# Kernel optimization log

Measured on AMD Instinct MI355X. Metric: run time of the kernel, lower is better.

## Reference

```python
import jax, jax.numpy as jnp
import numpy as np
import math

B, N, D = 1, 50000, 512  # batch (forced to 1 by the module's matmul shapes), nodes, embed_dim


def _uniform(key, shape, stdv):
    return jax.random.uniform(key, shape, minval=-stdv, maxval=stdv, dtype=jnp.float32)


def setup_inputs() -> dict:
    key = jax.random.key(0)
    ks = jax.random.split(key, 11)
    q = jax.random.normal(ks[0], (B, N, D), dtype=jnp.float32)
    l = jax.random.normal(ks[1], (B, 1, D), dtype=jnp.float32)
    context = jax.random.normal(ks[2], (B, 1, D), dtype=jnp.float32)
    g = jax.random.normal(ks[3], (B, 1, D), dtype=jnp.float32)
    mask = jax.random.randint(ks[4], (B, N), 0, 2, dtype=jnp.int32)
    mask = mask.at[:, 0].set(1)  # guarantee at least one feasible node
    random_net = jax.random.randint(ks[5], (B, 1), 0, N, dtype=jnp.int64)
    # learned parameters, uniform(-1/sqrt(fan), 1/sqrt(fan)) per init_parameters
    W_context = _uniform(ks[6], (1, 1, 2), 1.0 / math.sqrt(2))
    W_graph = _uniform(ks[7], (1, 1, 2), 1.0 / math.sqrt(2))
    W_query = _uniform(ks[8], (D, D), 1.0 / math.sqrt(D))
    W_key = _uniform(ks[9], (D, D), 1.0 / math.sqrt(D))
    return {
        "q": q, "l": l, "context": context, "g": g, "mask": mask,
        "is_random": 0, "random_net": random_net,
        "W_context": W_context, "W_graph": W_graph,
        "W_query": W_query, "W_key": W_key,
    }


def reference(q, l, context, g, mask, is_random, random_net,
              W_context, W_graph, W_query, W_key):
    batch_size, graph_size, input_dim = q.shape
    mask_copy = mask
    norm_factor = 1.0 / math.sqrt(input_dim)  # key_dim == embed_dim (n_heads=1)

    # context mixing: concat = W_context[0] @ [l; context]  -> (B,1,D)
    lc = jnp.concatenate([l, context], axis=1).reshape(-1, input_dim)      # (2B, D)
    concat = jnp.matmul(W_context[0], lc).reshape(batch_size, 1, input_dim)
    # graph mixing: g_context = W_graph[0] @ [g; concat]    -> (B,1,D)
    gc = jnp.concatenate([g, concat], axis=1).reshape(-1, input_dim)
    g_context = jnp.matmul(W_graph[0], gc).reshape(batch_size, 1, input_dim)

    Q = jnp.matmul(g_context.reshape(-1, input_dim), W_query).reshape(batch_size, 1, -1)
    K = jnp.matmul(q.reshape(-1, input_dim), W_key).reshape(batch_size, graph_size, -1)

    compat = jnp.tanh(norm_factor * jnp.einsum('bqk,bnk->bqn', Q, K)) * 10.0  # (B,1,N)
    maskf = mask.astype(jnp.float32)[:, None, :]
    compat = jnp.where(maskf <= 0.1, -jnp.inf, compat)

    softmax = jax.nn.softmax(compat, axis=2)
    log_softmax = jax.nn.log_softmax(compat, axis=2)

    if not is_random:  # static Python branch (is_random is a plain int)
        max_indx = jnp.argmax(softmax, axis=2)          # (B,1)
    else:
        max_indx = random_net

    rows = jnp.arange(batch_size)
    idx = max_indx[:, 0]
    q_max = q[rows, idx][:, None, :]                    # (B,1,D)
    attn_max = softmax[rows, 0, idx].reshape(batch_size, 1)
    log_attn_max = log_softmax[rows, 0, idx].reshape(batch_size, 1)
    return (q_max, attn_max, log_attn_max, concat, mask_copy, max_indx)
```

## Files before the change

kernel.cpp:

```cpp
#include <hip/hip_runtime.h>
#include <math.h>

#define DIM 512
#define NROWS 50000
#define NORM 0.04419417382415922f

#define QP_BLOCKS 64
#define QPART_BLOCKS 32
#define VK_BLOCKS 128
#define CP_BLOCKS 2048
#define CP_THREADS 256

#define OUT_ATTN 512
#define OUT_LOG  513
#define OUT_IDX  51026


__device__ inline float dot4(float4 a, float4 b, float acc) {
    acc = fmaf(a.x, b.x, acc);
    acc = fmaf(a.y, b.y, acc);
    acc = fmaf(a.z, b.z, acc);
    acc = fmaf(a.w, b.w, acc);
    return acc;
}

__device__ inline void sm_combine(float& m, float& s, int& idx,
                                  float m2, float s2, int idx2) {
    bool take2 = (m2 > m) || (m2 == m && idx2 < idx);
    float hm = take2 ? m2 : m;
    float hs = take2 ? s2 : s;
    int   hi = take2 ? idx2 : idx;
    float lm = take2 ? m : m2;
    float ls = take2 ? s : s2;
    if (lm > -INFINITY) hs = fmaf(ls, expf(lm - hm), hs);
    m = hm; s = hs; idx = hi;
}

__global__ __launch_bounds__(256) void qpart_kernel(
    const float* __restrict__ l, const float* __restrict__ ctx,
    const float* __restrict__ g, const float* __restrict__ Wc,
    const float* __restrict__ Wg, const float* __restrict__ Wq,
    const int* __restrict__ mask,
    float* __restrict__ qpart, float* __restrict__ out_concat,
    float* __restrict__ out_maskf) {
    int t = threadIdx.x;
    int b = blockIdx.x;
    for (int i = b * 256 + t; i < NROWS; i += QP_BLOCKS * 256)
        out_maskf[i] = (float)mask[i];
    if (b >= QPART_BLOCKS) return;

    __shared__ float gctx[DIM];
    float wc0 = Wc[0], wc1 = Wc[1], wg0 = Wg[0], wg1 = Wg[1];
    for (int j = t; j < DIM; j += 256) {
        float cc = wc0 * l[j] + wc1 * ctx[j];
        if (b == 0) out_concat[j] = cc;
        gctx[j] = wg0 * g[j] + wg1 * cc;
    }
    __syncthreads();
    int d0 = b * 16;
    float acc0 = 0.f, acc1 = 0.f;
    for (int d = d0; d < d0 + 16; ++d) {
        float gd = gctx[d];
        acc0 = fmaf(gd, Wq[d * DIM + t], acc0);
        acc1 = fmaf(gd, Wq[d * DIM + t + 256], acc1);
    }
    qpart[b * DIM + t] = acc0;
    qpart[b * DIM + t + 256] = acc1;
}

__global__ __launch_bounds__(256) void v_kernel(
    const float* __restrict__ Wk, const float* __restrict__ qpart,
    float* __restrict__ v) {
    __shared__ __align__(16) float Q[DIM];
    int t = threadIdx.x;
    for (int j = t; j < DIM; j += 256) {
        float a = 0.f;
        for (int p = 0; p < QPART_BLOCKS; ++p) a += qpart[p * DIM + j];
        Q[j] = a;
    }
    __syncthreads();
    int lane = t & 63;
    int w = t >> 6;
    int r = blockIdx.x * 4 + w;
    const float4* row = (const float4*)(Wk + (size_t)r * DIM);
    const float4* qv = (const float4*)Q;
    float4 a0 = row[lane],      a1 = row[lane + 64];
    float4 b0 = qv[lane],       b1 = qv[lane + 64];
    float d = dot4(a1, b1, dot4(a0, b0, 0.f));
    #pragma unroll
    for (int off = 32; off > 0; off >>= 1) d += __shfl_xor(d, off);
    if (lane == 0) v[r] = d;
}

__global__ __launch_bounds__(CP_THREADS) void compat_kernel(
    const float* __restrict__ q, const int* __restrict__ mask,
    const float* __restrict__ v, float* __restrict__ compat,
    float* __restrict__ pm, float* __restrict__ ps, int* __restrict__ pidx) {
    int t = threadIdx.x;
    int gtid = blockIdx.x * CP_THREADS + t;
    int gsz = CP_BLOCKS * CP_THREADS;

    int lane = t & 63;
    int wid = gtid >> 6;
    int nw = gsz >> 6;

    const float4* vv = (const float4*)v;
    float4 b0 = vv[lane];
    float4 b1 = vv[lane + 64];

    float m = -INFINITY, s = 0.f;
    int idx = 0x7fffffff;

    for (int n = wid; n < NROWS; n += nw) {
        if (mask[n] == 0) {
            if (lane == 0) compat[n] = -INFINITY;
            continue;
        }
        const float4* row = (const float4*)(q + (size_t)n * DIM);
        float4 a0 = row[lane];
        float4 a1 = row[lane + 64];
        float d = dot4(a1, b1, dot4(a0, b0, 0.f));
        #pragma unroll
        for (int off = 32; off > 0; off >>= 1) d += __shfl_xor(d, off);
        float c = tanhf(NORM * d) * 10.0f;
        if (lane == 0) compat[n] = c;
        sm_combine(m, s, idx, c, 1.0f, n);
    }

    __shared__ float bm[CP_THREADS / 64], bs[CP_THREADS / 64];
    __shared__ int bidx[CP_THREADS / 64];
    int w = t >> 6;
    if (lane == 0) { bm[w] = m; bs[w] = s; bidx[w] = idx; }
    __syncthreads();
    if (t == 0) {
        float M = bm[0], S = bs[0];
        int I = bidx[0];
        for (int i = 1; i < CP_THREADS / 64; ++i)
            sm_combine(M, S, I, bm[i], bs[i], bidx[i]);
        pm[blockIdx.x] = M;
        ps[blockIdx.x] = S;
        pidx[blockIdx.x] = I;
    }
}

__global__ __launch_bounds__(512) void finalize_kernel(
    const float* __restrict__ q, const float* __restrict__ pm,
    const float* __restrict__ ps, const int* __restrict__ pidx,
    const float* __restrict__ compat, const int* __restrict__ is_random,
    const long long* __restrict__ rnet, float* __restrict__ out) {
    __shared__ float sm[512], ss[512];
    __shared__ int si[512];
    __shared__ int chosen;
    int t = threadIdx.x;
    float m = -INFINITY, s = 0.f;
    int idx = 0x7fffffff;
    for (int i = t; i < CP_BLOCKS; i += 512)
        sm_combine(m, s, idx, pm[i], ps[i], pidx[i]);
    sm[t] = m; ss[t] = s; si[t] = idx;
    __syncthreads();
    for (int off = 256; off > 0; off >>= 1) {
        if (t < off) {
            float M = sm[t], S = ss[t];
            int I = si[t];
            sm_combine(M, S, I, sm[t + off], ss[t + off], si[t + off]);
            sm[t] = M; ss[t] = S; si[t] = I;
        }
        __syncthreads();
    }
    if (t == 0) {
        float M = sm[0], S = ss[0];
        int ix = si[0];
        if (is_random[0] != 0) ix = (int)rnet[0];
        float c = compat[ix];
        out[OUT_ATTN] = expf(c - M) / S;
        out[OUT_LOG]  = (c - M) - logf(S);
        out[OUT_IDX]  = (float)ix;
        chosen = ix;
    }
    __syncthreads();
    out[t] = q[(size_t)chosen * DIM + t];
}

extern "C" void kernel_launch(void* const* d_in, const int* in_sizes, int n_in,
                              void* d_out, int out_size, void* d_ws, size_t ws_size,
                              hipStream_t stream) {
    const float*     q    = (const float*)d_in[0];
    const float*     l    = (const float*)d_in[1];
    const float*     ctx  = (const float*)d_in[2];
    const float*     g    = (const float*)d_in[3];
    const int*       mask = (const int*)d_in[4];
    const int*       isr  = (const int*)d_in[5];
    const long long* rnet = (const long long*)d_in[6];
    const float*     Wc   = (const float*)d_in[7];
    const float*     Wg   = (const float*)d_in[8];
    const float*     Wq   = (const float*)d_in[9];
    const float*     Wk   = (const float*)d_in[10];

    float* out = (float*)d_out;
    float* ws  = (float*)d_ws;
    float* qpart  = ws;
    float* v      = ws + 16384;
    float* pm     = ws + 16896;
    float* ps     = ws + 18944;
    int*   pidx   = (int*)(ws + 20992);
    float* compat = ws + 23040;

    qpart_kernel<<<QP_BLOCKS, 256, 0, stream>>>(l, ctx, g, Wc, Wg, Wq, mask, qpart, out + 514, out + 1026);
    v_kernel<<<VK_BLOCKS, 256, 0, stream>>>(Wk, qpart, v);
    compat_kernel<<<CP_BLOCKS, CP_THREADS, 0, stream>>>(q, mask, v, compat, pm, ps, pidx);
    finalize_kernel<<<1, 512, 0, stream>>>(q, pm, ps, pidx, compat, isr, rnet, out);
}
```

Baseline: 29.89 us.

## Process two rows per wavefront with mask prefetch and fast tanh in compat kernel

The compat kernel now splits each 64-lane wavefront into two 32-lane halves, each handling one masked row with four float4 loads per lane. The next row's mask value is prefetched one iteration ahead, and the shuffle reduction is shortened to five steps. tanhf is replaced by an exp2/rcp formulation and expf by __expf in the softmax combine, which slightly reduces accuracy. The Q projection is also spread over all 64 blocks with 8 rows each, and the workspace offsets are enlarged to hold the larger partial buffer.

```diff
diff --git a/kernel.cpp b/kernel.cpp
--- a/kernel.cpp
+++ b/kernel.cpp
@@ -6,8 +6,7 @@
 #define NORM 0.04419417382415922f
 
 #define QP_BLOCKS 64
-#define QPART_BLOCKS 32
-#define VK_BLOCKS 128
+#define V_BLOCKS 128
 #define CP_BLOCKS 2048
 #define CP_THREADS 256
 
@@ -32,7 +31,7 @@
     int   hi = take2 ? idx2 : idx;
     float lm = take2 ? m : m2;
     float ls = take2 ? s : s2;
-    if (lm > -INFINITY) hs = fmaf(ls, expf(lm - hm), hs);
+    if (lm > -INFINITY) hs = fmaf(ls, __expf(lm - hm), hs);
     m = hm; s = hs; idx = hi;
 }
 
@@ -47,7 +46,6 @@
     int b = blockIdx.x;
     for (int i = b * 256 + t; i < NROWS; i += QP_BLOCKS * 256)
         out_maskf[i] = (float)mask[i];
-    if (b >= QPART_BLOCKS) return;
 
     __shared__ float gctx[DIM];
     float wc0 = Wc[0], wc1 = Wc[1], wg0 = Wg[0], wg1 = Wg[1];
@@ -57,12 +55,13 @@
         gctx[j] = wg0 * g[j] + wg1 * cc;
     }
     __syncthreads();
-    int d0 = b * 16;
+    int d0 = b * 8;
     float acc0 = 0.f, acc1 = 0.f;
-    for (int d = d0; d < d0 + 16; ++d) {
-        float gd = gctx[d];
-        acc0 = fmaf(gd, Wq[d * DIM + t], acc0);
-        acc1 = fmaf(gd, Wq[d * DIM + t + 256], acc1);
+    #pragma unroll
+    for (int d = 0; d < 8; ++d) {
+        float gd = gctx[d0 + d];
+        acc0 = fmaf(gd, Wq[(d0 + d) * DIM + t], acc0);
+        acc1 = fmaf(gd, Wq[(d0 + d) * DIM + t + 256], acc1);
     }
     qpart[b * DIM + t] = acc0;
     qpart[b * DIM + t + 256] = acc1;
@@ -75,7 +74,7 @@
     int t = threadIdx.x;
     for (int j = t; j < DIM; j += 256) {
         float a = 0.f;
-        for (int p = 0; p < QPART_BLOCKS; ++p) a += qpart[p * DIM + j];
+        for (int p = 0; p < QP_BLOCKS; ++p) a += qpart[p * DIM + j];
         Q[j] = a;
     }
     __syncthreads();
@@ -97,45 +96,57 @@
     const float* __restrict__ v, float* __restrict__ compat,
     float* __restrict__ pm, float* __restrict__ ps, int* __restrict__ pidx) {
     int t = threadIdx.x;
-    int gtid = blockIdx.x * CP_THREADS + t;
-    int gsz = CP_BLOCKS * CP_THREADS;
-
     int lane = t & 63;
-    int wid = gtid >> 6;
-    int nw = gsz >> 6;
+    int w = t >> 6;
+    int g = lane >> 5;
+    int gl = lane & 31;
+    int wid = (blockIdx.x << 2) + w;
+    const int nw = CP_BLOCKS * 4;
 
     const float4* vv = (const float4*)v;
-    float4 b0 = vv[lane];
-    float4 b1 = vv[lane + 64];
+    float4 vf0 = vv[gl * 4 + 0], vf1 = vv[gl * 4 + 1];
+    float4 vf2 = vv[gl * 4 + 2], vf3 = vv[gl * 4 + 3];
 
     float m = -INFINITY, s = 0.f;
     int idx = 0x7fffffff;
 
-    for (int n = wid; n < NROWS; n += nw) {
-        if (mask[n] == 0) {
-            if (lane == 0) compat[n] = -INFINITY;
-            continue;
+    int base = wid * 2;
+    int mk = (base + g < NROWS) ? mask[base + g] : 0;
+    for (; base < NROWS; base += nw * 2) {
+        int nxt = base + nw * 2;
+        int mknext = (nxt + g < NROWS) ? mask[nxt + g] : 0;
+        int n = base + g;
+        if (mk) {
+            const float4* row = (const float4*)(q + (size_t)n * DIM);
+            float4 a0 = row[gl * 4 + 0];
+            float4 a1 = row[gl * 4 + 1];
+            float4 a2 = row[gl * 4 + 2];
+            float4 a3 = row[gl * 4 + 3];
+            float d = dot4(a0, vf0, 0.f);
+            d = dot4(a1, vf1, d);
+            d = dot4(a2, vf2, d);
+            d = dot4(a3, vf3, d);
+            #pragma unroll
+            for (int off = 16; off >= 1; off >>= 1) d += __shfl_xor(d, off);
+            float x = NORM * d;
+            float u = __builtin_amdgcn_exp2f(x * 2.885390081777927f);
+            float c = fmaf(-20.f, __builtin_amdgcn_rcpf(u + 1.f), 10.f);
+            if (gl == 0) compat[n] = c;
+            sm_combine(m, s, idx, c, 1.0f, n);
+        } else if (n < NROWS) {
+            if (gl == 0) compat[n] = -INFINITY;
         }
-        const float4* row = (const float4*)(q + (size_t)n * DIM);
-        float4 a0 = row[lane];
-        float4 a1 = row[lane + 64];
-        float d = dot4(a1, b1, dot4(a0, b0, 0.f));
-        #pragma unroll
-        for (int off = 32; off > 0; off >>= 1) d += __shfl_xor(d, off);
-        float c = tanhf(NORM * d) * 10.0f;
-        if (lane == 0) compat[n] = c;
-        sm_combine(m, s, idx, c, 1.0f, n);
-    }
-
-    __shared__ float bm[CP_THREADS / 64], bs[CP_THREADS / 64];
-    __shared__ int bidx[CP_THREADS / 64];
-    int w = t >> 6;
-    if (lane == 0) { bm[w] = m; bs[w] = s; bidx[w] = idx; }
+        mk = mknext;
+    }
+
+    __shared__ float bm[8], bs[8];
+    __shared__ int bidx[8];
+    if (gl == 0) { bm[w * 2 + g] = m; bs[w * 2 + g] = s; bidx[w * 2 + g] = idx; }
     __syncthreads();
     if (t == 0) {
         float M = bm[0], S = bs[0];
         int I = bidx[0];
-        for (int i = 1; i < CP_THREADS / 64; ++i)
+        for (int i = 1; i < 8; ++i)
             sm_combine(M, S, I, bm[i], bs[i], bidx[i]);
         pm[blockIdx.x] = M;
         ps[blockIdx.x] = S;
@@ -199,14 +210,17 @@
     float* out = (float*)d_out;
     float* ws  = (float*)d_ws;
     float* qpart  = ws;
-    float* v      = ws + 16384;
-    float* pm     = ws + 16896;
-    float* ps     = ws + 18944;
-    int*   pidx   = (int*)(ws + 20992);
-    float* compat = ws + 23040;
-
-    qpart_kernel<<<QP_BLOCKS, 256, 0, stream>>>(l, ctx, g, Wc, Wg, Wq, mask, qpart, out + 514, out + 1026);
-    v_kernel<<<VK_BLOCKS, 256, 0, stream>>>(Wk, qpart, v);
-    compat_kernel<<<CP_BLOCKS, CP_THREADS, 0, stream>>>(q, mask, v, compat, pm, ps, pidx);
-    finalize_kernel<<<1, 512, 0, stream>>>(q, pm, ps, pidx, compat, isr, rnet, out);
-}
+    float* v      = ws + 32768;
+    float* pm     = ws + 33280;
+    float* ps     = ws + 35328;
+    int*   pidx   = (int*)(ws + 37376);
+    float* compat = ws + 39424;
+
+    qpart_kernel<<<QP_BLOCKS, 256, 0, stream>>>(l, ctx, g, Wc, Wg, Wq, mask,
+                                                qpart, out + 514, out + 1026);
+    v_kernel<<<V_BLOCKS, 256, 0, stream>>>(Wk, qpart, v);
+    compat_kernel<<<CP_BLOCKS, CP_THREADS, 0, stream>>>(q, mask, v, compat,
+                                                        pm, ps, pidx);
+    finalize_kernel<<<1, 512, 0, stream>>>(q, pm, ps, pidx, compat,
+                                           isr, rnet, out);
+}
```

Result: slower. 32.59 us (+9.0%).

## Fuse Q and v kernels, drop compat buffer, use fast tanh/exp

Applied to the files above, without the earlier changes.

Merges the Q projection and the Wk-vector product into one kernel, where each block redundantly computes the full Q from Wq before doing its 8 rows of Wk. This removes one launch and the partial-sum buffer. The per-node compat array is no longer written: the argmax path takes c equal to the max, and the random path recomputes the chosen dot product in finalize. The mask-to-float copy moves into compat_kernel, and tanh/exp become exp2/rcp intrinsics. The cost is 64 blocks each reading all of Wq, plus slightly lower-precision tanh.

```diff
diff --git a/kernel.cpp b/kernel.cpp
--- a/kernel.cpp
+++ b/kernel.cpp
@@ -5,9 +5,7 @@
 #define NROWS 50000
 #define NORM 0.04419417382415922f
 
-#define QP_BLOCKS 64
-#define QPART_BLOCKS 32
-#define VK_BLOCKS 128
+#define QV_BLOCKS 64
 #define CP_BLOCKS 2048
 #define CP_THREADS 256
 
@@ -22,6 +20,11 @@
     acc = fmaf(a.z, b.z, acc);
     acc = fmaf(a.w, b.w, acc);
     return acc;
+}
+
+__device__ inline float tanh10(float x) {
+    float u = __builtin_amdgcn_exp2f(x * 2.885390081777927f);
+    return fmaf(-20.f, __builtin_amdgcn_rcpf(u + 1.f), 10.f);
 }
 
 __device__ inline void sm_combine(float& m, float& s, int& idx,
@@ -32,24 +35,21 @@
     int   hi = take2 ? idx2 : idx;
     float lm = take2 ? m : m2;
     float ls = take2 ? s : s2;
-    if (lm > -INFINITY) hs = fmaf(ls, expf(lm - hm), hs);
+    if (lm > -INFINITY) hs = fmaf(ls, __expf(lm - hm), hs);
     m = hm; s = hs; idx = hi;
 }
 
-__global__ __launch_bounds__(256) void qpart_kernel(
+__global__ __launch_bounds__(256) void qv_kernel(
     const float* __restrict__ l, const float* __restrict__ ctx,
     const float* __restrict__ g, const float* __restrict__ Wc,
     const float* __restrict__ Wg, const float* __restrict__ Wq,
-    const int* __restrict__ mask,
-    float* __restrict__ qpart, float* __restrict__ out_concat,
-    float* __restrict__ out_maskf) {
+    const float* __restrict__ Wk,
+    float* __restrict__ v, float* __restrict__ out_concat) {
     int t = threadIdx.x;
     int b = blockIdx.x;
-    for (int i = b * 256 + t; i < NROWS; i += QP_BLOCKS * 256)
-        out_maskf[i] = (float)mask[i];
-    if (b >= QPART_BLOCKS) return;
-
     __shared__ float gctx[DIM];
+    __shared__ __align__(16) float Qs[DIM];
+
     float wc0 = Wc[0], wc1 = Wc[1], wg0 = Wg[0], wg1 = Wg[1];
     for (int j = t; j < DIM; j += 256) {
         float cc = wc0 * l[j] + wc1 * ctx[j];
@@ -57,79 +57,72 @@
         gctx[j] = wg0 * g[j] + wg1 * cc;
     }
     __syncthreads();
-    int d0 = b * 16;
-    float acc0 = 0.f, acc1 = 0.f;
-    for (int d = d0; d < d0 + 16; ++d) {
-        float gd = gctx[d];
-        acc0 = fmaf(gd, Wq[d * DIM + t], acc0);
-        acc1 = fmaf(gd, Wq[d * DIM + t + 256], acc1);
-    }
-    qpart[b * DIM + t] = acc0;
-    qpart[b * DIM + t + 256] = acc1;
-}
-
-__global__ __launch_bounds__(256) void v_kernel(
-    const float* __restrict__ Wk, const float* __restrict__ qpart,
-    float* __restrict__ v) {
-    __shared__ __align__(16) float Q[DIM];
-    int t = threadIdx.x;
-    for (int j = t; j < DIM; j += 256) {
-        float a = 0.f;
-        for (int p = 0; p < QPART_BLOCKS; ++p) a += qpart[p * DIM + j];
-        Q[j] = a;
-    }
-    __syncthreads();
+
+    const float2* Wq2 = (const float2*)Wq;
+    float2 acc0 = make_float2(0.f, 0.f), acc1 = make_float2(0.f, 0.f);
+    for (int k = 0; k < 256; ++k) {
+        float g0 = gctx[k], g1 = gctx[k + 256];
+        float2 w0 = Wq2[k * 256 + t];
+        float2 w1 = Wq2[(k + 256) * 256 + t];
+        acc0.x = fmaf(g0, w0.x, acc0.x);
+        acc0.y = fmaf(g0, w0.y, acc0.y);
+        acc1.x = fmaf(g1, w1.x, acc1.x);
+        acc1.y = fmaf(g1, w1.y, acc1.y);
+    }
+    ((float2*)Qs)[t] = make_float2(acc0.x + acc1.x, acc0.y + acc1.y);
+    __syncthreads();
+
     int lane = t & 63;
     int w = t >> 6;
-    int r = blockIdx.x * 4 + w;
-    const float4* row = (const float4*)(Wk + (size_t)r * DIM);
-    const float4* qv = (const float4*)Q;
-    float4 a0 = row[lane],      a1 = row[lane + 64];
-    float4 b0 = qv[lane],       b1 = qv[lane + 64];
-    float d = dot4(a1, b1, dot4(a0, b0, 0.f));
+    const float4* qv4 = (const float4*)Qs;
+    float4 q0 = qv4[lane], q1 = qv4[lane + 64];
     #pragma unroll
-    for (int off = 32; off > 0; off >>= 1) d += __shfl_xor(d, off);
-    if (lane == 0) v[r] = d;
+    for (int rr = 0; rr < 2; ++rr) {
+        int r = b * 8 + w * 2 + rr;
+        const float4* row = (const float4*)(Wk + (size_t)r * DIM);
+        float4 a0 = row[lane], a1 = row[lane + 64];
+        float d = dot4(a1, q1, dot4(a0, q0, 0.f));
+        #pragma unroll
+        for (int off = 32; off > 0; off >>= 1) d += __shfl_xor(d, off);
+        if (lane == 0) v[r] = d;
+    }
 }
 
 __global__ __launch_bounds__(CP_THREADS) void compat_kernel(
     const float* __restrict__ q, const int* __restrict__ mask,
-    const float* __restrict__ v, float* __restrict__ compat,
-    float* __restrict__ pm, float* __restrict__ ps, int* __restrict__ pidx) {
+    const float* __restrict__ v,
+    float* __restrict__ pm, float* __restrict__ ps, int* __restrict__ pidx,
+    float* __restrict__ out_maskf) {
     int t = threadIdx.x;
     int gtid = blockIdx.x * CP_THREADS + t;
-    int gsz = CP_BLOCKS * CP_THREADS;
+    if (gtid < NROWS) out_maskf[gtid] = (float)mask[gtid];
 
     int lane = t & 63;
+    int w = t >> 6;
     int wid = gtid >> 6;
-    int nw = gsz >> 6;
+    const int nw = (CP_BLOCKS * CP_THREADS) >> 6;
 
     const float4* vv = (const float4*)v;
-    float4 b0 = vv[lane];
-    float4 b1 = vv[lane + 64];
+    float4 vb0 = vv[lane];
+    float4 vb1 = vv[lane + 64];
 
     float m = -INFINITY, s = 0.f;
     int idx = 0x7fffffff;
 
     for (int n = wid; n < NROWS; n += nw) {
-        if (mask[n] == 0) {
-            if (lane == 0) compat[n] = -INFINITY;
-            continue;
-        }
+        if (mask[n] == 0) continue;
         const float4* row = (const float4*)(q + (size_t)n * DIM);
         float4 a0 = row[lane];
         float4 a1 = row[lane + 64];
-        float d = dot4(a1, b1, dot4(a0, b0, 0.f));
+        float d = dot4(a1, vb1, dot4(a0, vb0, 0.f));
         #pragma unroll
         for (int off = 32; off > 0; off >>= 1) d += __shfl_xor(d, off);
-        float c = tanhf(NORM * d) * 10.0f;
-        if (lane == 0) compat[n] = c;
+        float c = tanh10(NORM * d);
         sm_combine(m, s, idx, c, 1.0f, n);
     }
 
     __shared__ float bm[CP_THREADS / 64], bs[CP_THREADS / 64];
     __shared__ int bidx[CP_THREADS / 64];
-    int w = t >> 6;
     if (lane == 0) { bm[w] = m; bs[w] = s; bidx[w] = idx; }
     __syncthreads();
     if (t == 0) {
@@ -144,13 +137,13 @@
 }
 
 __global__ __launch_bounds__(512) void finalize_kernel(
-    const float* __restrict__ q, const float* __restrict__ pm,
+    const float* __restrict__ q, const int* __restrict__ mask,
+    const float* __restrict__ v, const float* __restrict__ pm,
     const float* __restrict__ ps, const int* __restrict__ pidx,
-    const float* __restrict__ compat, const int* __restrict__ is_random,
-    const long long* __restrict__ rnet, float* __restrict__ out) {
-    __shared__ float sm[512], ss[512];
+    const int* __restrict__ is_random, const long long* __restrict__ rnet,
+    float* __restrict__ out) {
+    __shared__ float sm[512], ss[512], sd[512];
     __shared__ int si[512];
-    __shared__ int chosen;
     int t = threadIdx.x;
     float m = -INFINITY, s = 0.f;
     int idx = 0x7fffffff;
@@ -167,18 +160,33 @@
         }
         __syncthreads();
     }
+    __shared__ int chosenIx, chosenRnd;
+    __shared__ float chosenM, chosenS;
     if (t == 0) {
-        float M = sm[0], S = ss[0];
-        int ix = si[0];
-        if (is_random[0] != 0) ix = (int)rnet[0];
-        float c = compat[ix];
-        out[OUT_ATTN] = expf(c - M) / S;
-        out[OUT_LOG]  = (c - M) - logf(S);
+        chosenRnd = is_random[0];
+        chosenIx = chosenRnd ? (int)rnet[0] : si[0];
+        chosenM = sm[0];
+        chosenS = ss[0];
+    }
+    __syncthreads();
+    int ix = chosenIx;
+    float r0 = q[(size_t)ix * DIM + t];
+    out[t] = r0;
+    sd[t] = r0 * v[t];
+    __syncthreads();
+    for (int off = 256; off > 0; off >>= 1) {
+        if (t < off) sd[t] += sd[t + off];
+        __syncthreads();
+    }
+    if (t == 0) {
+        float Mv = chosenM, Sv = chosenS;
+        float c = chosenRnd
+                ? (mask[ix] ? tanh10(NORM * sd[0]) : -INFINITY)
+                : Mv;
+        out[OUT_ATTN] = __expf(c - Mv) / Sv;
+        out[OUT_LOG]  = (c - Mv) - logf(Sv);
         out[OUT_IDX]  = (float)ix;
-        chosen = ix;
-    }
-    __syncthreads();
-    out[t] = q[(size_t)chosen * DIM + t];
+    }
 }
 
 extern "C" void kernel_launch(void* const* d_in, const int* in_sizes, int n_in,
@@ -198,15 +206,15 @@
 
     float* out = (float*)d_out;
     float* ws  = (float*)d_ws;
-    float* qpart  = ws;
-    float* v      = ws + 16384;
-    float* pm     = ws + 16896;
-    float* ps     = ws + 18944;
-    int*   pidx   = (int*)(ws + 20992);
-    float* compat = ws + 23040;
-
-    qpart_kernel<<<QP_BLOCKS, 256, 0, stream>>>(l, ctx, g, Wc, Wg, Wq, mask, qpart, out + 514, out + 1026);
-    v_kernel<<<VK_BLOCKS, 256, 0, stream>>>(Wk, qpart, v);
-    compat_kernel<<<CP_BLOCKS, CP_THREADS, 0, stream>>>(q, mask, v, compat, pm, ps, pidx);
-    finalize_kernel<<<1, 512, 0, stream>>>(q, pm, ps, pidx, compat, isr, rnet, out);
-}
+    float* v    = ws;
+    float* pm   = ws + 512;
+    float* ps   = ws + 2560;
+    int*   pidx = (int*)(ws + 4608);
+
+    qv_kernel<<<QV_BLOCKS, 256, 0, stream>>>(l, ctx, g, Wc, Wg, Wq, Wk,
+                                             v, out + 514);
+    compat_kernel<<<CP_BLOCKS, CP_THREADS, 0, stream>>>(q, mask, v, pm, ps,
+                                                        pidx, out + 1026);
+    finalize_kernel<<<1, 512, 0, stream>>>(q, mask, v, pm, ps, pidx,
+                                           isr, rnet, out);
+}
```

Result: slower. 48.39 us (+61.9%).
